# Kernel tuning notes

Hardware: AMD Instinct MI355X
Metric: run time of the kernel (lower is better)

The kernel has to match this reference:

```python
import jax, jax.numpy as jnp
import numpy as np

P, I, H, A = 4096, 256, 64, 32  # num_person, num_item, hidden_dim, latent_dim


def _linear_params(key, fan_in, fan_out):
    # xavier-normal-ish init; exact init values don't matter for correctness baseline
    kw, _ = jax.random.split(key)
    w = jax.random.normal(kw, (fan_in, fan_out), jnp.float32) * (1.0 / np.sqrt(fan_in))
    b = jnp.zeros((fan_out,), jnp.float32)
    return w, b


def setup_inputs() -> dict:
    key = jax.random.key(0)
    ks = jax.random.split(key, 12)
    response = jax.random.uniform(ks[0], (P, I, 1), jnp.float32)
    mask = jax.random.randint(ks[1], (P, I, 1), 0, 2).astype(jnp.int32)
    item_index = jnp.arange(I, dtype=jnp.int32).reshape(I, 1)
    eps_ability = jax.random.normal(ks[2], (P, A), jnp.float32)
    eps_item = jax.random.normal(ks[3], (I, 1), jnp.float32)
    # ability encoder (mean merge): mlp1 = Lin(1,H), ELU, Lin(H,H); then extra ELU
    w1, b1 = _linear_params(ks[4], 1, H)
    w2, b2 = _linear_params(ks[5], H, H)
    # mlp2 = Lin(H,H), ELU, Lin(H, 2*A)
    w3, b3 = _linear_params(ks[6], H, H)
    w4, b4 = _linear_params(ks[7], H, 2 * A)
    # item encoder: mu/logvar embedding tables, item_feat_dim=1 for 1PL
    mu_table = jax.random.normal(ks[8], (I, 1), jnp.float32)
    logvar_table = jax.random.normal(ks[9], (I, 1), jnp.float32) * 0.1 - 1.0
    return dict(response=response, mask=mask, item_index=item_index,
                eps_ability=eps_ability, eps_item=eps_item,
                w1=w1, b1=b1, w2=w2, b2=b2, w3=w3, b3=b3, w4=w4, b4=b4,
                mu_table=mu_table, logvar_table=logvar_table)


def reference(response, mask, item_index, eps_ability, eps_item,
              w1, b1, w2, b2, w3, b3, w4, b4, mu_table, logvar_table):
    elu = jax.nn.elu
    num_person, num_item, _ = response.shape
    # --- ability encoder, mean merge ---
    x = response.reshape(num_person * num_item, 1)
    h = elu(elu(x @ w1 + b1) @ w2 + b2)            # extra ELU per _forward_mean
    h = h.reshape(num_person, num_item, H)
    m = mask.astype(h.dtype)                        # [P, I, 1]
    # masked mean over each person's observed items (fused segmented reduction)
    denom = jnp.maximum(m.sum(axis=1), 1.0)         # [P, 1] (guard; mask never all-zero)
    hid_mean = (h * m).sum(axis=1) / denom          # [P, H]
    out = elu(hid_mean @ w3 + b3) @ w4 + b4         # [P, 2A]
    ability_mu, ability_logvar = out[:, :A], out[:, A:]
    # --- item encoder: embedding lookups ---
    idx = item_index.squeeze(1)
    item_mu = mu_table[idx]                         # [I, 1]
    item_logvar = logvar_table[idx]
    # --- reparameterize ---
    ability = ability_mu + eps_ability * jnp.exp(0.5 * ability_logvar)
    item_feat = item_mu + eps_item * jnp.exp(0.5 * item_logvar)
    # --- 1PL IRT decoder ---
    logit = ability.sum(axis=1, keepdims=True) + item_feat.T   # [P, I]
    response_mu = jax.nn.sigmoid(logit)[..., None]             # [P, I, 1]
    return response_mu, ability_mu, ability_logvar, item_mu, item_logvar
```

## Files before the change

### kernel.cpp

```cpp
#include <hip/hip_runtime.h>
#include <hip/hip_bf16.h>

#define PN 4096
#define IN 256
#define HN 64
#define AN 32

#define OFF_RESP 0
#define OFF_AMU  (PN * IN)
#define OFF_ALV  (OFF_AMU + PN * AN)
#define OFF_IMU  (OFF_ALV + PN * AN)
#define OFF_ILV  (OFF_IMU + IN)

#define TROWS 128
#define PERS  8

typedef short  s16x8  __attribute__((ext_vector_type(8)));
typedef float  f32x4  __attribute__((ext_vector_type(4)));

__device__ __forceinline__ unsigned short f2bf(float f) {
    union { float f; unsigned int u; } v; v.f = f;
    unsigned int u = v.u;
    u += 0x7FFFu + ((u >> 16) & 1u);
    return (unsigned short)(u >> 16);
}

__device__ __forceinline__ float eluf(float x) {
    return x > 0.0f ? x : (__expf(x) - 1.0f);
}

__device__ __forceinline__ unsigned int pack_bf16(float a, float b) {
    union { __hip_bfloat162 h; unsigned int u; } cv;
    cv.h = __float22bfloat162_rn(make_float2(a, b));
    return cv.u;
}

__global__ __launch_bounds__(256, 2) void k_fused(
    const float* __restrict__ response,
    const int* __restrict__ mask,
    const float* __restrict__ w1,
    const float* __restrict__ b1,
    const float* __restrict__ w2,
    const float* __restrict__ b2,
    const float* __restrict__ w3,
    const float* __restrict__ b3,
    const float* __restrict__ w4,
    const float* __restrict__ b4,
    const float* __restrict__ eps_ability,
    const int* __restrict__ item_index,
    const float* __restrict__ eps_item,
    const float* __restrict__ mu_table,
    const float* __restrict__ logvar_table,
    float* __restrict__ out_amu,
    float* __restrict__ out_alv,
    float* __restrict__ out_imu,
    float* __restrict__ out_ilv,
    float* __restrict__ out_resp)
{
    __shared__ __align__(16) unsigned char sRegA[27648];
    __shared__ float sW[PERS * 132];
    __shared__ __align__(16) unsigned short sWB[16 * 136];
    __shared__ __align__(16) unsigned short sW3T[64 * 72];
    __shared__ __align__(16) unsigned short sW4T[64 * 72];
    __shared__ float sW1[64], sB1[64], sB2[64], sB3[64], sB4[64];
    __shared__ float sIF[256];
    __shared__ int   sCnt[16];
    __shared__ float sAS[PERS];

    unsigned short* sH1  = (unsigned short*)sRegA;
    unsigned short* sW2T = (unsigned short*)sRegA + 128 * 72;
    unsigned short* sTB  = (unsigned short*)sRegA;
    unsigned short* sHMB = (unsigned short*)sRegA;
    unsigned short* sT2  = (unsigned short*)sRegA + 16 * 72;
    float*          sOut = (float*)(sRegA + 2 * 16 * 72 * 2);

    const int t    = threadIdx.x;
    const int p0   = blockIdx.x * PERS;
    const int wave = t >> 6;
    const int lane = t & 63;
    const int quad = lane >> 4;
    const int r    = lane & 15;

    if (t < 64) {
        sW1[t] = w1[t]; sB1[t] = b1[t]; sB2[t] = b2[t];
        sB3[t] = b3[t]; sB4[t] = b4[t];
    }
    for (int base = t * 4; base < 4096; base += 1024) {
        int j = base >> 6, n0 = base & 63;
        float4 v2 = *(const float4*)&w2[base];
        sW2T[(n0 + 0) * 72 + j] = f2bf(v2.x);
        sW2T[(n0 + 1) * 72 + j] = f2bf(v2.y);
        sW2T[(n0 + 2) * 72 + j] = f2bf(v2.z);
        sW2T[(n0 + 3) * 72 + j] = f2bf(v2.w);
        float4 v3 = *(const float4*)&w3[base];
        sW3T[(n0 + 0) * 72 + j] = f2bf(v3.x);
        sW3T[(n0 + 1) * 72 + j] = f2bf(v3.y);
        sW3T[(n0 + 2) * 72 + j] = f2bf(v3.z);
        sW3T[(n0 + 3) * 72 + j] = f2bf(v3.w);
        float4 v4 = *(const float4*)&w4[base];
        sW4T[(n0 + 0) * 72 + j] = f2bf(v4.x);
        sW4T[(n0 + 1) * 72 + j] = f2bf(v4.y);
        sW4T[(n0 + 2) * 72 + j] = f2bf(v4.z);
        sW4T[(n0 + 3) * 72 + j] = f2bf(v4.w);
    }
    {
        int idx = item_index[t];
        float mu = mu_table[idx];
        float lv = logvar_table[idx];
        sIF[t] = mu + eps_item[t] * __expf(0.5f * lv);
        if (blockIdx.x == 0) { out_imu[t] = mu; out_ilv[t] = lv; }
    }
    for (int idx = t; idx < PERS * 132; idx += 256) sW[idx] = 0.0f;
    for (int idx = t; idx < 16 * 68; idx += 256) ((unsigned int*)sWB)[idx] = 0u;
    if (t < 16) sCnt[t] = 0;
    __syncthreads();

    {
        int row  = t & 127;
        int half = t >> 7;
        float xg = (float)row * (1.0f / 127.0f);
        #pragma unroll
        for (int j0 = half * 32; j0 < half * 32 + 32; j0 += 8) {
            uint4 pk;
            pk.x = pack_bf16(eluf(fmaf(xg, sW1[j0+0], sB1[j0+0])),
                             eluf(fmaf(xg, sW1[j0+1], sB1[j0+1])));
            pk.y = pack_bf16(eluf(fmaf(xg, sW1[j0+2], sB1[j0+2])),
                             eluf(fmaf(xg, sW1[j0+3], sB1[j0+3])));
            pk.z = pack_bf16(eluf(fmaf(xg, sW1[j0+4], sB1[j0+4])),
                             eluf(fmaf(xg, sW1[j0+5], sB1[j0+5])));
            pk.w = pack_bf16(eluf(fmaf(xg, sW1[j0+6], sB1[j0+6])),
                             eluf(fmaf(xg, sW1[j0+7], sB1[j0+7])));
            *(uint4*)&sH1[row * 72 + j0] = pk;
        }
    }

    #pragma unroll
    for (int k = 0; k < 2; ++k) {
        int vi = t + 256 * k;
        float4 xr = ((const float4*)(response + p0 * IN))[vi];
        int4   mr = ((const int4*)(mask + p0 * IN))[vi];
        int person = (t >> 6) + 4 * k;
        unsigned long long b0 = __ballot(mr.x != 0);
        unsigned long long b1 = __ballot(mr.y != 0);
        unsigned long long b2 = __ballot(mr.z != 0);
        unsigned long long b3 = __ballot(mr.w != 0);
        if (lane == 0)
            sCnt[person] = (int)(__popcll(b0) + __popcll(b1) + __popcll(b2) + __popcll(b3));
        float xs[4] = {xr.x, xr.y, xr.z, xr.w};
        int   ms[4] = {mr.x, mr.y, mr.z, mr.w};
        #pragma unroll
        for (int u = 0; u < 4; ++u) {
            if (ms[u]) {
                float kf = xs[u] * 127.0f;
                int kk = (int)kf;
                kk = (kk < 0) ? 0 : ((kk > 126) ? 126 : kk);
                float w = kf - (float)kk;
                atomicAdd(&sW[person * 132 + kk],     1.0f - w);
                atomicAdd(&sW[person * 132 + kk + 1], w);
            }
        }
    }
    __syncthreads();

    f32x4 accT[2][4];
    #pragma unroll
    for (int rt = 0; rt < 2; ++rt)
        #pragma unroll
        for (int ct = 0; ct < 4; ++ct)
            accT[rt][ct] = (f32x4){0.f, 0.f, 0.f, 0.f};
    #pragma unroll
    for (int kk = 0; kk < 64; kk += 32) {
        s16x8 af[2], bfr[4];
        #pragma unroll
        for (int rt = 0; rt < 2; ++rt)
            af[rt] = *(const s16x8*)&sH1[(wave * 32 + rt * 16 + r) * 72 + kk + quad * 8];
        #pragma unroll
        for (int ct = 0; ct < 4; ++ct)
            bfr[ct] = *(const s16x8*)&sW2T[(ct * 16 + r) * 72 + kk + quad * 8];
        #pragma unroll
        for (int rt = 0; rt < 2; ++rt)
            #pragma unroll
            for (int ct = 0; ct < 4; ++ct)
                accT[rt][ct] = __builtin_amdgcn_mfma_f32_16x16x32_bf16(
                    af[rt], bfr[ct], accT[rt][ct], 0, 0, 0);
    }
    __syncthreads();

    #pragma unroll
    for (int ct = 0; ct < 4; ++ct) {
        int col = ct * 16 + r;
        float bb = sB2[col];
        #pragma unroll
        for (int rt = 0; rt < 2; ++rt)
            #pragma unroll
            for (int reg = 0; reg < 4; ++reg) {
                int krow = wave * 32 + rt * 16 + quad * 4 + reg;
                sTB[col * 136 + krow] = f2bf(eluf(accT[rt][ct][reg] + bb));
            }
    }
    #pragma unroll
    for (int idx = t; idx < PERS * 64; idx += 256) {
        int row = idx >> 6, kp = (idx & 63) * 2;
        ((unsigned int*)sWB)[row * 68 + (idx & 63)] =
            pack_bf16(sW[row * 132 + kp], sW[row * 132 + kp + 1]);
    }
    __syncthreads();

    f32x4 accH = (f32x4){0.f, 0.f, 0.f, 0.f};
    #pragma unroll
    for (int s = 0; s < 4; ++s) {
        s16x8 af = *(const s16x8*)&sWB[r * 136 + s * 32 + quad * 8];
        s16x8 bfr = *(const s16x8*)&sTB[(wave * 16 + r) * 136 + s * 32 + quad * 8];
        accH = __builtin_amdgcn_mfma_f32_16x16x32_bf16(af, bfr, accH, 0, 0, 0);
    }
    __syncthreads();

    {
        int col = wave * 16 + r;
        #pragma unroll
        for (int reg = 0; reg < 4; ++reg) {
            int person = quad * 4 + reg;
            float c = fmaxf((float)sCnt[person], 1.0f);
            sHMB[person * 72 + col] = f2bf(accH[reg] / c);
        }
    }
    __syncthreads();

    f32x4 accA = (f32x4){0.f, 0.f, 0.f, 0.f};
    #pragma unroll
    for (int kk = 0; kk < 64; kk += 32) {
        s16x8 af = *(const s16x8*)&sHMB[r * 72 + kk + quad * 8];
        s16x8 bfr = *(const s16x8*)&sW3T[(wave * 16 + r) * 72 + kk + quad * 8];
        accA = __builtin_amdgcn_mfma_f32_16x16x32_bf16(af, bfr, accA, 0, 0, 0);
    }
    {
        int col = wave * 16 + r;
        float bb = sB3[col];
        #pragma unroll
        for (int reg = 0; reg < 4; ++reg)
            sT2[(quad * 4 + reg) * 72 + col] = f2bf(eluf(accA[reg] + bb));
    }
    __syncthreads();

    f32x4 accB = (f32x4){0.f, 0.f, 0.f, 0.f};
    #pragma unroll
    for (int kk = 0; kk < 64; kk += 32) {
        s16x8 af = *(const s16x8*)&sT2[r * 72 + kk + quad * 8];
        s16x8 bfr = *(const s16x8*)&sW4T[(wave * 16 + r) * 72 + kk + quad * 8];
        accB = __builtin_amdgcn_mfma_f32_16x16x32_bf16(af, bfr, accB, 0, 0, 0);
    }
    {
        int col = wave * 16 + r;
        float bb = sB4[col];
        #pragma unroll
        for (int reg = 0; reg < 4; ++reg)
            sOut[(quad * 4 + reg) * 68 + col] = accB[reg] + bb;
    }
    __syncthreads();

    {
        int pl = t >> 5, a = t & 31;
        float mu = sOut[pl * 68 + a];
        float lv = sOut[pl * 68 + a + 32];
        out_amu[(p0 + pl) * AN + a] = mu;
        out_alv[(p0 + pl) * AN + a] = lv;
        float partial = mu + eps_ability[(p0 + pl) * AN + a] * __expf(0.5f * lv);
        #pragma unroll
        for (int off = 16; off; off >>= 1) partial += __shfl_xor(partial, off);
        if (a == 0) sAS[pl] = partial;
    }
    __syncthreads();

    #pragma unroll
    for (int k3 = 0; k3 < 2; ++k3) {
        int vi = t + 256 * k3;
        int pl = vi >> 6, i0 = (vi & 63) * 4;
        float a = sAS[pl];
        f32x4 pk;
        #pragma unroll
        for (int u = 0; u < 4; ++u)
            pk[u] = 1.0f / (1.0f + __expf(-(a + sIF[i0 + u])));
        *(f32x4*)&out_resp[(p0 + pl) * IN + i0] = pk;
    }
}

extern "C" void kernel_launch(void* const* d_in, const int* in_sizes, int n_in,
                              void* d_out, int out_size, void* d_ws, size_t ws_size,
                              hipStream_t stream)
{
    const float* response     = (const float*)d_in[0];
    const int*   mask         = (const int*)d_in[1];
    const int*   item_index   = (const int*)d_in[2];
    const float* eps_ability  = (const float*)d_in[3];
    const float* eps_item     = (const float*)d_in[4];
    const float* w1           = (const float*)d_in[5];
    const float* b1           = (const float*)d_in[6];
    const float* w2           = (const float*)d_in[7];
    const float* b2           = (const float*)d_in[8];
    const float* w3           = (const float*)d_in[9];
    const float* b3           = (const float*)d_in[10];
    const float* w4           = (const float*)d_in[11];
    const float* b4           = (const float*)d_in[12];
    const float* mu_table     = (const float*)d_in[13];
    const float* logvar_table = (const float*)d_in[14];

    float* out = (float*)d_out;

    k_fused<<<PN / PERS, 256, 0, stream>>>(
        response, mask, w1, b1, w2, b2, w3, b3, w4, b4,
        eps_ability, item_index, eps_item, mu_table, logvar_table,
        out + OFF_AMU, out + OFF_ALV, out + OFF_IMU, out + OFF_ILV,
        out + OFF_RESP);
}
```

Baseline: 97.90 us.

## Remove sync barriers by computing final MLP layer redundantly per wave with shuffles

Global loads of response, mask, eps and item tables are hoisted to kernel start so their latency overlaps with weight staging. The separate bf16 repack of histogram weights is dropped; each lane converts fp32 rows to bf16 directly into MFMA operands, which removes one barrier. The last layer is computed redundantly by every wave across all four column tiles, and the per-person ability sums are reduced with cross-lane shuffles instead of shared-memory staging, removing two more barriers. This adds redundant MFMA work and register pressure in exchange for fewer synchronization points.

```diff
diff --git a/kernel.cpp b/kernel.cpp
--- a/kernel.cpp
+++ b/kernel.cpp
@@ -58,21 +58,18 @@
     float* __restrict__ out_resp)
 {
     __shared__ __align__(16) unsigned char sRegA[27648];
-    __shared__ float sW[PERS * 132];
-    __shared__ __align__(16) unsigned short sWB[16 * 136];
+    __shared__ __align__(16) float sW[16 * 132];
     __shared__ __align__(16) unsigned short sW3T[64 * 72];
     __shared__ __align__(16) unsigned short sW4T[64 * 72];
     __shared__ float sW1[64], sB1[64], sB2[64], sB3[64], sB4[64];
     __shared__ float sIF[256];
     __shared__ int   sCnt[16];
-    __shared__ float sAS[PERS];
 
     unsigned short* sH1  = (unsigned short*)sRegA;
     unsigned short* sW2T = (unsigned short*)sRegA + 128 * 72;
     unsigned short* sTB  = (unsigned short*)sRegA;
-    unsigned short* sHMB = (unsigned short*)sRegA;
-    unsigned short* sT2  = (unsigned short*)sRegA + 16 * 72;
-    float*          sOut = (float*)(sRegA + 2 * 16 * 72 * 2);
+    unsigned short* sHMB = (unsigned short*)(sRegA + 17408);
+    unsigned short* sT2  = (unsigned short*)(sRegA + 19712);
 
     const int t    = threadIdx.x;
     const int p0   = blockIdx.x * PERS;
@@ -80,6 +77,27 @@
     const int lane = t & 63;
     const int quad = lane >> 4;
     const int r    = lane & 15;
+
+    float4 xr[2];
+    int4   mr[2];
+    #pragma unroll
+    for (int k = 0; k < 2; ++k) {
+        int vi = t + 256 * k;
+        xr[k] = ((const float4*)(response + p0 * IN))[vi];
+        mr[k] = ((const int4*)(mask + p0 * IN))[vi];
+    }
+    float epsv[4][2] = {{0.f,0.f},{0.f,0.f},{0.f,0.f},{0.f,0.f}};
+    if (quad < 2) {
+        #pragma unroll
+        for (int reg = 0; reg < 4; ++reg)
+            #pragma unroll
+            for (int ct = 0; ct < 2; ++ct)
+                epsv[reg][ct] = eps_ability[(p0 + quad * 4 + reg) * AN + ct * 16 + r];
+    }
+    int   ii_idx = item_index[t];
+    float ii_mu  = mu_table[ii_idx];
+    float ii_lv  = logvar_table[ii_idx];
+    float ii_eps = eps_item[t];
 
     if (t < 64) {
         sW1[t] = w1[t]; sB1[t] = b1[t]; sB2[t] = b2[t];
@@ -104,14 +122,10 @@
         sW4T[(n0 + 3) * 72 + j] = f2bf(v4.w);
     }
     {
-        int idx = item_index[t];
-        float mu = mu_table[idx];
-        float lv = logvar_table[idx];
-        sIF[t] = mu + eps_item[t] * __expf(0.5f * lv);
-        if (blockIdx.x == 0) { out_imu[t] = mu; out_ilv[t] = lv; }
-    }
-    for (int idx = t; idx < PERS * 132; idx += 256) sW[idx] = 0.0f;
-    for (int idx = t; idx < 16 * 68; idx += 256) ((unsigned int*)sWB)[idx] = 0u;
+        sIF[t] = ii_mu + ii_eps * __expf(0.5f * ii_lv);
+        if (blockIdx.x == 0) { out_imu[t] = ii_mu; out_ilv[t] = ii_lv; }
+    }
+    for (int idx = t; idx < 16 * 132; idx += 256) sW[idx] = 0.0f;
     if (t < 16) sCnt[t] = 0;
     __syncthreads();
 
@@ -136,18 +150,15 @@
 
     #pragma unroll
     for (int k = 0; k < 2; ++k) {
-        int vi = t + 256 * k;
-        float4 xr = ((const float4*)(response + p0 * IN))[vi];
-        int4   mr = ((const int4*)(mask + p0 * IN))[vi];
-        int person = (t >> 6) + 4 * k;
-        unsigned long long b0 = __ballot(mr.x != 0);
-        unsigned long long b1 = __ballot(mr.y != 0);
-        unsigned long long b2 = __ballot(mr.z != 0);
-        unsigned long long b3 = __ballot(mr.w != 0);
+        int person = wave + 4 * k;
+        unsigned long long bl0 = __ballot(mr[k].x != 0);
+        unsigned long long bl1 = __ballot(mr[k].y != 0);
+        unsigned long long bl2 = __ballot(mr[k].z != 0);
+        unsigned long long bl3 = __ballot(mr[k].w != 0);
         if (lane == 0)
-            sCnt[person] = (int)(__popcll(b0) + __popcll(b1) + __popcll(b2) + __popcll(b3));
-        float xs[4] = {xr.x, xr.y, xr.z, xr.w};
-        int   ms[4] = {mr.x, mr.y, mr.z, mr.w};
+            sCnt[person] = (int)(__popcll(bl0) + __popcll(bl1) + __popcll(bl2) + __popcll(bl3));
+        float xs[4] = {xr[k].x, xr[k].y, xr[k].z, xr[k].w};
+        int   ms[4] = {mr[k].x, mr[k].y, mr[k].z, mr[k].w};
         #pragma unroll
         for (int u = 0; u < 4; ++u) {
             if (ms[u]) {
@@ -198,22 +209,27 @@
                 sTB[col * 136 + krow] = f2bf(eluf(accT[rt][ct][reg] + bb));
             }
     }
-    #pragma unroll
-    for (int idx = t; idx < PERS * 64; idx += 256) {
-        int row = idx >> 6, kp = (idx & 63) * 2;
-        ((unsigned int*)sWB)[row * 68 + (idx & 63)] =
-            pack_bf16(sW[row * 132 + kp], sW[row * 132 + kp + 1]);
-    }
-    __syncthreads();
-
+    __syncthreads();
+
+    s16x8 afW[4];
+    #pragma unroll
+    for (int s = 0; s < 4; ++s) {
+        const float* src = &sW[r * 132 + s * 32 + quad * 8];
+        f32x4 lo = *(const f32x4*)src;
+        f32x4 hi = *(const f32x4*)(src + 4);
+        union { s16x8 v; unsigned int u[4]; } o;
+        o.u[0] = pack_bf16(lo[0], lo[1]);
+        o.u[1] = pack_bf16(lo[2], lo[3]);
+        o.u[2] = pack_bf16(hi[0], hi[1]);
+        o.u[3] = pack_bf16(hi[2], hi[3]);
+        afW[s] = o.v;
+    }
     f32x4 accH = (f32x4){0.f, 0.f, 0.f, 0.f};
     #pragma unroll
     for (int s = 0; s < 4; ++s) {
-        s16x8 af = *(const s16x8*)&sWB[r * 136 + s * 32 + quad * 8];
         s16x8 bfr = *(const s16x8*)&sTB[(wave * 16 + r) * 136 + s * 32 + quad * 8];
-        accH = __builtin_amdgcn_mfma_f32_16x16x32_bf16(af, bfr, accH, 0, 0, 0);
-    }
-    __syncthreads();
+        accH = __builtin_amdgcn_mfma_f32_16x16x32_bf16(afW[s], bfr, accH, 0, 0, 0);
+    }
 
     {
         int col = wave * 16 + r;
@@ -242,40 +258,75 @@
     }
     __syncthreads();
 
-    f32x4 accB = (f32x4){0.f, 0.f, 0.f, 0.f};
-    #pragma unroll
-    for (int kk = 0; kk < 64; kk += 32) {
-        s16x8 af = *(const s16x8*)&sT2[r * 72 + kk + quad * 8];
-        s16x8 bfr = *(const s16x8*)&sW4T[(wave * 16 + r) * 72 + kk + quad * 8];
-        accB = __builtin_amdgcn_mfma_f32_16x16x32_bf16(af, bfr, accB, 0, 0, 0);
-    }
-    {
-        int col = wave * 16 + r;
-        float bb = sB4[col];
-        #pragma unroll
-        for (int reg = 0; reg < 4; ++reg)
-            sOut[(quad * 4 + reg) * 68 + col] = accB[reg] + bb;
-    }
-    __syncthreads();
-
-    {
-        int pl = t >> 5, a = t & 31;
-        float mu = sOut[pl * 68 + a];
-        float lv = sOut[pl * 68 + a + 32];
-        out_amu[(p0 + pl) * AN + a] = mu;
-        out_alv[(p0 + pl) * AN + a] = lv;
-        float partial = mu + eps_ability[(p0 + pl) * AN + a] * __expf(0.5f * lv);
-        #pragma unroll
-        for (int off = 16; off; off >>= 1) partial += __shfl_xor(partial, off);
-        if (a == 0) sAS[pl] = partial;
-    }
-    __syncthreads();
+    s16x8 afT[2];
+    afT[0] = *(const s16x8*)&sT2[r * 72 + 0  + quad * 8];
+    afT[1] = *(const s16x8*)&sT2[r * 72 + 32 + quad * 8];
+    f32x4 accB0 = (f32x4){0.f,0.f,0.f,0.f};
+    f32x4 accB1 = (f32x4){0.f,0.f,0.f,0.f};
+    f32x4 accB2 = (f32x4){0.f,0.f,0.f,0.f};
+    f32x4 accB3 = (f32x4){0.f,0.f,0.f,0.f};
+    #pragma unroll
+    for (int kk = 0; kk < 2; ++kk) {
+        s16x8 b0 = *(const s16x8*)&sW4T[(0 * 16 + r) * 72 + kk * 32 + quad * 8];
+        s16x8 b1 = *(const s16x8*)&sW4T[(1 * 16 + r) * 72 + kk * 32 + quad * 8];
+        s16x8 b2v = *(const s16x8*)&sW4T[(2 * 16 + r) * 72 + kk * 32 + quad * 8];
+        s16x8 b3v = *(const s16x8*)&sW4T[(3 * 16 + r) * 72 + kk * 32 + quad * 8];
+        accB0 = __builtin_amdgcn_mfma_f32_16x16x32_bf16(afT[kk], b0,  accB0, 0, 0, 0);
+        accB1 = __builtin_amdgcn_mfma_f32_16x16x32_bf16(afT[kk], b1,  accB1, 0, 0, 0);
+        accB2 = __builtin_amdgcn_mfma_f32_16x16x32_bf16(afT[kk], b2v, accB2, 0, 0, 0);
+        accB3 = __builtin_amdgcn_mfma_f32_16x16x32_bf16(afT[kk], b3v, accB3, 0, 0, 0);
+    }
+    float b4v0 = sB4[0 * 16 + r];
+    float b4v1 = sB4[1 * 16 + r];
+    float b4v2 = sB4[2 * 16 + r];
+    float b4v3 = sB4[3 * 16 + r];
+
+    {
+        f32x4 my = accB0; float bmy = b4v0;
+        if (wave == 1) { my = accB1; bmy = b4v1; }
+        else if (wave == 2) { my = accB2; bmy = b4v2; }
+        else if (wave == 3) { my = accB3; bmy = b4v3; }
+        if (quad < 2) {
+            float* dst = (wave < 2) ? out_amu : out_alv;
+            int a = (wave & 1) * 16 + r;
+            #pragma unroll
+            for (int reg = 0; reg < 4; ++reg)
+                dst[(p0 + quad * 4 + reg) * AN + a] = my[reg] + bmy;
+        }
+    }
+    float S0, S1, S2, S3;
+    {
+        float mu0, mu1, lv0, lv1;
+        mu0 = accB0[0] + b4v0; mu1 = accB1[0] + b4v1;
+        lv0 = accB2[0] + b4v2; lv1 = accB3[0] + b4v3;
+        S0 = mu0 + epsv[0][0] * __expf(0.5f * lv0) + mu1 + epsv[0][1] * __expf(0.5f * lv1);
+        mu0 = accB0[1] + b4v0; mu1 = accB1[1] + b4v1;
+        lv0 = accB2[1] + b4v2; lv1 = accB3[1] + b4v3;
+        S1 = mu0 + epsv[1][0] * __expf(0.5f * lv0) + mu1 + epsv[1][1] * __expf(0.5f * lv1);
+        mu0 = accB0[2] + b4v0; mu1 = accB1[2] + b4v1;
+        lv0 = accB2[2] + b4v2; lv1 = accB3[2] + b4v3;
+        S2 = mu0 + epsv[2][0] * __expf(0.5f * lv0) + mu1 + epsv[2][1] * __expf(0.5f * lv1);
+        mu0 = accB0[3] + b4v0; mu1 = accB1[3] + b4v1;
+        lv0 = accB2[3] + b4v2; lv1 = accB3[3] + b4v3;
+        S3 = mu0 + epsv[3][0] * __expf(0.5f * lv0) + mu1 + epsv[3][1] * __expf(0.5f * lv1);
+    }
+    #pragma unroll
+    for (int off = 1; off < 16; off <<= 1) {
+        S0 += __shfl_xor(S0, off);
+        S1 += __shfl_xor(S1, off);
+        S2 += __shfl_xor(S2, off);
+        S3 += __shfl_xor(S3, off);
+    }
+    float pw = S0;
+    if (wave == 1) pw = S1;
+    else if (wave == 2) pw = S2;
+    else if (wave == 3) pw = S3;
 
     #pragma unroll
     for (int k3 = 0; k3 < 2; ++k3) {
-        int vi = t + 256 * k3;
-        int pl = vi >> 6, i0 = (vi & 63) * 4;
-        float a = sAS[pl];
+        int pl = wave + 4 * k3;
+        float a = __shfl(pw, k3 * 16);
+        int i0 = lane * 4;
         f32x4 pk;
         #pragma unroll
         for (int u = 0; u < 4; ++u)
```

New measurement: 99.91 us. 2.0% more time.
